# Kernel tuning notes

Measured on AMD Instinct MI355X. Metric: run time of the kernel, lower is better.

## Reference

```python
import jax, jax.numpy as jnp
import numpy as np

EPS = 1e-5
H, HD = 8, 32  # n_heads, head_dim


def layer_norm(x, w, b):
    mu = jnp.mean(x, axis=-1, keepdims=True)
    var = jnp.mean(jnp.square(x - mu), axis=-1, keepdims=True)
    return (x - mu) * jax.lax.rsqrt(var + EPS) * w + b


def setup_inputs() -> dict:
    key = jax.random.key(0)
    ks = jax.random.split(key, 6)
    S, N, Dm, Dz = 256, 512, 64, 128
    return {
        "m": jax.random.normal(ks[0], (1, S, N, Dm), jnp.float32),
        "z": jax.random.normal(ks[1], (1, N, N, Dz), jnp.float32),
        "m_norm_w": jnp.ones((Dm,), jnp.float32),
        "m_norm_b": jnp.zeros((Dm,), jnp.float32),
        "z_norm_w": jnp.ones((Dz,), jnp.float32),
        "z_norm_b": jnp.zeros((Dz,), jnp.float32),
        "Wm": jax.random.normal(ks[2], (Dm, H * HD), jnp.float32) * 0.05,
        "Wg": jax.random.normal(ks[3], (Dm, H * HD), jnp.float32) * 0.05,
        "Wz": jax.random.normal(ks[4], (Dz, H), jnp.float32) * 0.05,
        "Wo": jax.random.normal(ks[5], (H * HD, Dm), jnp.float32) * 0.05,
    }


def reference(m, z, m_norm_w, m_norm_b, z_norm_w, z_norm_b, Wm, Wg, Wz, Wo):
    m0 = m[0]  # [S, N, Dm]
    z0 = z[0]  # [N, N, Dz]
    Dm = m0.shape[-1]
    mn = layer_norm(m0, m_norm_w, m_norm_b)
    zn = layer_norm(z0, z_norm_w, z_norm_b)
    # per-head softmax bias from pair rep: b[h,i,j]
    b = jnp.einsum('ijc,ch->hij', zn, Wz)
    w = jax.nn.softmax(b, axis=-1)  # [H, N, N]
    # values and gates: [S, N, H, HD]
    v = jnp.einsum('snc,chk->snhk', mn, Wm.reshape(Dm, H, HD))
    g = jax.nn.sigmoid(jnp.einsum('snc,chk->snhk', mn, Wg.reshape(Dm, H, HD)))
    # weighted averaging over tokens j
    o = jnp.einsum('hij,sjhk->sihk', w, v)  # [S, N, H, HD]
    out = jnp.einsum('sihk,hkc->sic', o * g, Wo.reshape(H, HD, Dm))
    return out[None]  # [1, S, N, Dm]
```

## Files before the change

### kernel.cpp

```cpp
#include <hip/hip_runtime.h>


#define S_DIM 256
#define N_DIM 512
#define DM 64
#define DZ 128
#define NH 8
#define HD 32
#define HK 256
#define NP 8192
#define BKP 32
#define JT_N 16

typedef unsigned int   u32;
typedef unsigned short u16;
typedef __bf16 bf16x8 __attribute__((ext_vector_type(8)));
typedef float  f32x4  __attribute__((ext_vector_type(4)));
typedef u32    u32x4  __attribute__((ext_vector_type(4)));

__device__ __forceinline__ u16 f2bf(float f) {
  u32 u = __builtin_bit_cast(u32, f);
  return (u16)((u + 0x7FFFu + ((u >> 16) & 1u)) >> 16);
}
__device__ __forceinline__ float bf2f(u16 h) {
  u32 u = ((u32)h) << 16;
  return __builtin_bit_cast(float, u);
}
__device__ __forceinline__ u32 pack2(float a, float b) {
  return (u32)f2bf(a) | ((u32)f2bf(b) << 16);
}
__device__ __forceinline__ bf16x8 ld8(const u16* p) {
  return __builtin_bit_cast(bf16x8, *(const u32x4*)p);
}
__device__ __forceinline__ f32x4 mfma16(bf16x8 a, bf16x8 b, f32x4 c) {
  return __builtin_amdgcn_mfma_f32_16x16x32_bf16(a, b, c, 0, 0, 0);
}
__device__ __forceinline__ void gload_lds16(const void* gsrc, void* ldst) {
  __builtin_amdgcn_global_load_lds(
      (const __attribute__((address_space(1))) void*)gsrc,
      (__attribute__((address_space(3))) void*)ldst, 16, 0, 0);
}
__device__ __forceinline__ float fast_sigmoid(float x) {
  float r;
  asm("v_rcp_f32 %0, %1" : "=v"(r) : "v"(1.f + __expf(-x)));
  return r;
}
__device__ __forceinline__ int swz(int lin) { return lin ^ (((lin >> 7) & 3) << 4); }

#define BARRIER() do { asm volatile("" ::: "memory"); \
                       __builtin_amdgcn_s_barrier();  \
                       asm volatile("" ::: "memory"); } while (0)

__global__ __launch_bounds__(256) void k0_prep(
    const float* __restrict__ Wm, const float* __restrict__ Wg,
    const float* __restrict__ Wo, const float* __restrict__ znw,
    const float* __restrict__ znb, const float* __restrict__ Wz,
    u16* __restrict__ wmg, u16* __restrict__ wof,
    u16* __restrict__ wzf, float* __restrict__ t1c) {
  const int idx = blockIdx.x * 256 + threadIdx.x;
  if (idx < 32768) {
    const int t = idx & 7, lane = (idx >> 3) & 63, ks = (idx >> 9) & 1, cb = idx >> 10;
    const int c = cb * 16 + (lane & 15);
    const int k = ks * 32 + ((lane >> 4) & 3) * 8 + t;
    const float v = (c < HK) ? Wm[k * HK + c] : Wg[k * HK + (c - HK)];
    wmg[idx] = f2bf(v);
  } else if (idx < 32768 + 16384) {
    const int j = idx - 32768;
    const int t = j & 7, lane = (j >> 3) & 63, ks = (j >> 9) & 7, cb = j >> 12;
    const int c = cb * 16 + (lane & 15);
    const int hk = ks * 32 + ((lane >> 4) & 3) * 8 + t;
    wof[j] = f2bf(Wo[hk * DM + c]);
  } else if (idx < 49152 + 4096) {
    const int q = idx - 49152;
    const int t = q & 7, lane = (q >> 3) & 63, p = (q >> 9) & 1, ks = q >> 10;
    const int h = lane & 15;
    const int k = ks * 32 + ((lane >> 4) & 3) * 8 + t;
    u16 val = 0;
    if (h < NH) {
      const float wp = znw[k] * Wz[k * NH + h];
      const u16 hi = f2bf(wp);
      val = (p == 0) ? hi : f2bf(wp - bf2f(hi));
    }
    wzf[q] = val;
  } else if (idx < 49152 + 4096 + 16) {
    const int q = idx - 49152 - 4096;
    const int h = q & 7;
    float s = 0.f;
    for (int c = 0; c < DZ; ++c)
      s += ((q < 8) ? znw[c] : znb[c]) * Wz[c * NH + h];
    t1c[q] = s;
  }
}

__global__ __launch_bounds__(256) void k1a_bias(
    const float* __restrict__ z, const u16* __restrict__ wzf,
    const float* __restrict__ t1c, float* __restrict__ bws) {
  __shared__ float sB[NH][72];
  const int tid = threadIdx.x, lane = tid & 63, wv = tid >> 6;
  const int jb = blockIdx.x, i = blockIdx.y;
  const int jrow = jb * 64 + wv * 16 + (lane & 15);
  const float* zp = z + ((size_t)i * N_DIM + jrow) * DZ + ((lane >> 4) & 3) * 8;
  f32x4 acc = (f32x4){0.f, 0.f, 0.f, 0.f};
  float sum = 0.f, sq = 0.f;
  #pragma unroll
  for (int ks = 0; ks < 4; ++ks) {
    const float4 v0 = *(const float4*)(zp + ks * 32);
    const float4 v1 = *(const float4*)(zp + ks * 32 + 4);
    const float xs[8] = {v0.x, v0.y, v0.z, v0.w, v1.x, v1.y, v1.z, v1.w};
    bf16x8 zh, zl;
    #pragma unroll
    for (int t = 0; t < 8; ++t) {
      sum += xs[t]; sq += xs[t] * xs[t];
      const u16 h16 = f2bf(xs[t]);
      ((u16*)&zh)[t] = h16;
      ((u16*)&zl)[t] = f2bf(xs[t] - bf2f(h16));
    }
    const bf16x8 wh = ld8(wzf + (ks * 2 + 0) * 512 + lane * 8);
    const bf16x8 wl = ld8(wzf + (ks * 2 + 1) * 512 + lane * 8);
    acc = mfma16(zh, wh, acc);
    acc = mfma16(zl, wh, acc);
    acc = mfma16(zh, wl, acc);
  }
  sum += __shfl_xor(sum, 16, 64); sum += __shfl_xor(sum, 32, 64);
  sq  += __shfl_xor(sq, 16, 64);  sq  += __shfl_xor(sq, 32, 64);
  const float mu = sum * (1.f / DZ);
  const float rs = rsqrtf(sq * (1.f / DZ) - mu * mu + 1e-5f);
  const int h = lane & 15;
  const float t1 = t1c[h & 7], cst = t1c[8 + (h & 7)];
  #pragma unroll
  for (int rg = 0; rg < 4; ++rg) {
    const int r = ((lane >> 4) & 3) * 4 + rg;
    const float mur = __shfl(mu, r, 64);
    const float rsr = __shfl(rs, r, 64);
    const float bv = rsr * (acc[rg] - mur * t1) + cst;
    if (h < NH) sB[h][wv * 16 + r] = bv;
  }
  __syncthreads();
  #pragma unroll
  for (int q = 0; q < 2; ++q) {
    const int idx = tid + q * 256;
    const int hh = idx >> 6, jl = idx & 63;
    bws[((size_t)hh * N_DIM + i) * N_DIM + jb * 64 + jl] = sB[hh][jl];
  }
}

__global__ __launch_bounds__(256) void k1b_softmax(
    const float* __restrict__ bws, u16* __restrict__ wout) {
  const int tid = threadIdx.x, lane = tid & 63, wv = tid >> 6;
  const int row = blockIdx.x * 4 + wv;
  const int h = row >> 9, i = row & 511;
  const float* bp = bws + (size_t)row * N_DIM + lane * 8;
  const float4 v0 = *(const float4*)bp;
  const float4 v1 = *(const float4*)(bp + 4);
  float xs[8] = {v0.x, v0.y, v0.z, v0.w, v1.x, v1.y, v1.z, v1.w};
  float mx = xs[0];
  #pragma unroll
  for (int t = 1; t < 8; ++t) mx = fmaxf(mx, xs[t]);
  #pragma unroll
  for (int off = 32; off; off >>= 1) mx = fmaxf(mx, __shfl_xor(mx, off, 64));
  float sm = 0.f;
  #pragma unroll
  for (int t = 0; t < 8; ++t) { xs[t] = __expf(xs[t] - mx); sm += xs[t]; }
  #pragma unroll
  for (int off = 32; off; off >>= 1) sm += __shfl_xor(sm, off, 64);
  const float inv = 1.f / sm;
  u32x4 pk;
  pk[0] = pack2(xs[0] * inv, xs[1] * inv);
  pk[1] = pack2(xs[2] * inv, xs[3] * inv);
  pk[2] = pack2(xs[4] * inv, xs[5] * inv);
  pk[3] = pack2(xs[6] * inv, xs[7] * inv);
  *(u32x4*)(wout + (((size_t)(h * JT_N + (lane >> 2)) * N_DIM + i) << 5)
            + (lane & 3) * 8) = pk;
}

__global__ __launch_bounds__(256) void k2a_ln_m(
    const float* __restrict__ m, const float* __restrict__ mnw,
    const float* __restrict__ mnb, u16* __restrict__ mn) {
  __shared__ float sw[DM], sb[DM];
  const int tid = threadIdx.x;
  if (tid < DM) { sw[tid] = mnw[tid]; sb[tid] = mnb[tid]; }
  __syncthreads();
  const size_t r = (size_t)blockIdx.x * 256 + tid;
  const float4* mp = (const float4*)(m + r * DM);
  float4 arr[16];
  float sum = 0.f, sq = 0.f;
  #pragma unroll
  for (int q = 0; q < 16; ++q) {
    float4 v = mp[q]; arr[q] = v;
    sum += v.x + v.y + v.z + v.w;
    sq  += v.x * v.x + v.y * v.y + v.z * v.z + v.w * v.w;
  }
  const float mu = sum * (1.f / DM);
  const float rs = rsqrtf(sq * (1.f / DM) - mu * mu + 1e-5f);
  uint4* op = (uint4*)(mn + r * DM);
  #pragma unroll
  for (int q = 0; q < 8; ++q) {
    const float4 a = arr[2 * q], b = arr[2 * q + 1];
    const int c0 = q * 8;
    const float y0 = (a.x - mu) * rs * sw[c0 + 0] + sb[c0 + 0];
    const float y1 = (a.y - mu) * rs * sw[c0 + 1] + sb[c0 + 1];
    const float y2 = (a.z - mu) * rs * sw[c0 + 2] + sb[c0 + 2];
    const float y3 = (a.w - mu) * rs * sw[c0 + 3] + sb[c0 + 3];
    const float y4 = (b.x - mu) * rs * sw[c0 + 4] + sb[c0 + 4];
    const float y5 = (b.y - mu) * rs * sw[c0 + 5] + sb[c0 + 5];
    const float y6 = (b.z - mu) * rs * sw[c0 + 6] + sb[c0 + 6];
    const float y7 = (b.w - mu) * rs * sw[c0 + 7] + sb[c0 + 7];
    uint4 u;
    u.x = pack2(y0, y1); u.y = pack2(y2, y3);
    u.z = pack2(y4, y5); u.w = pack2(y6, y7);
    op[q] = u;
  }
}

__global__ __launch_bounds__(256) void k2b_proj(
    const u16* __restrict__ mn, const u16* __restrict__ wmg,
    u16* __restrict__ vf) {
  const int tid = threadIdx.x, lane = tid & 63, wv = tid >> 6;
  const int rbase = (blockIdx.x * 4 + wv) * 16;
  const u16* ap = mn + (size_t)(rbase + (lane & 15)) * DM + ((lane >> 4) & 3) * 8;
  const bf16x8 a0 = ld8(ap);
  const bf16x8 a1 = ld8(ap + 32);
  const u16* bp = wmg + lane * 8;
  const int r0 = rbase + ((lane >> 4) & 3) * 4;
  const int s0 = r0 >> 9;
  const int j0 = r0 & 511;

  f32x4 acc[16];
  #pragma unroll
  for (int cb = 0; cb < 16; ++cb) acc[cb] = (f32x4){0.f, 0.f, 0.f, 0.f};
  #pragma unroll
  for (int cb = 0; cb < 16; ++cb) {
    acc[cb] = mfma16(a0, ld8(bp + cb * 1024), acc[cb]);
    acc[cb] = mfma16(a1, ld8(bp + cb * 1024 + 512), acc[cb]);
  }
  #pragma unroll
  for (int cb = 0; cb < 16; ++cb) {
    const int c = cb * 16 + (lane & 15);
    const int h = c >> 5, k = c & 31;
    const int np = s0 * HD + k;
    const size_t idx = (((size_t)(h * JT_N + (j0 >> 5)) * NP + np) << 5) + (j0 & 31);
    ushort4 pk;
    pk.x = f2bf(acc[cb][0]); pk.y = f2bf(acc[cb][1]);
    pk.z = f2bf(acc[cb][2]); pk.w = f2bf(acc[cb][3]);
    *(ushort4*)(vf + idx) = pk;
  }
}

__global__ __launch_bounds__(256, 4) void k3_fused(
    const u16* __restrict__ wf, const u16* __restrict__ vf,
    const u16* __restrict__ mn, const u16* __restrict__ wmg,
    const u16* __restrict__ wof, float* __restrict__ out) {
  __shared__ __attribute__((aligned(16))) u16 ring[4][4096];
  const int tid = threadIdx.x, lane = tid & 63, wv = tid >> 6;
  const int q = (lane >> 4) & 3;
  const int wr = wv >> 1, wc = wv & 1;
  const int bid = blockIdx.x;
  const int xcd = bid & 7, j = bid >> 3;
  const int xt = xcd * 16 + (j >> 3);
  const int yt = j & 7;
  const int i0 = yt * 64;
  const int n0 = xt * 64;
  const int s  = xt * 2 + wc;

  const int sbA = wv * 1024;
  const int soA = swz(sbA + lane * 16);
  const int soB = swz(sbA + lane * 16);

  int offA[2], offB[2];
  #pragma unroll
  for (int f = 0; f < 2; ++f)
    offA[f] = swz((wr * 32 + f * 16 + (lane & 15)) * 64 + q * 16);
  #pragma unroll
  for (int f = 0; f < 2; ++f)
    offB[f] = 4096 + swz((wc * 32 + f * 16 + (lane & 15)) * 64 + q * 16);

  bf16x8 mnf[2][2];
  #pragma unroll
  for (int fi = 0; fi < 2; ++fi) {
    const u16* mp_ = mn + (size_t)(s * N_DIM + i0 + wr * 32 + fi * 16
                                   + (lane & 15)) * DM + q * 8;
    mnf[fi][0] = ld8(mp_);
    mnf[fi][1] = ld8(mp_ + 32);
  }

  f32x4 acc[2][2];
  f32x4 oacc[4][2];
  #pragma unroll
  for (int a = 0; a < 2; ++a)
    #pragma unroll
    for (int b = 0; b < 2; ++b) acc[a][b] = (f32x4){0.f, 0.f, 0.f, 0.f};
  #pragma unroll
  for (int a = 0; a < 4; ++a)
    #pragma unroll
    for (int b = 0; b < 2; ++b) oacc[a][b] = (f32x4){0.f, 0.f, 0.f, 0.f};

  const char* gA = (const char*)(wf + (size_t)i0 * 32);
  const char* gB = (const char*)(vf + (size_t)n0 * 32);

#define STAGE_P(pA_, pB_, slot)                                            \
  do {                                                                     \
    char* dA_ = (char*)&ring[(slot)][0];                                   \
    gload_lds16((pA_) + soA, dA_ + sbA);                                   \
    gload_lds16((pB_) + soB, dA_ + 4096 + sbA);                            \
  } while (0)

#define COMPUTE(slot)                                                      \
  do {                                                                     \
    const char* cS_ = (const char*)&ring[(slot)][0];                       \
    bf16x8 af_[2], bf_[2];                                                 \
    _Pragma("unroll")                                                      \
    for (int f = 0; f < 2; ++f) af_[f] = ld8((const u16*)(cS_ + offA[f])); \
    _Pragma("unroll")                                                      \
    for (int f = 0; f < 2; ++f) bf_[f] = ld8((const u16*)(cS_ + offB[f])); \
    __builtin_amdgcn_s_setprio(1);                                         \
    _Pragma("unroll")                                                      \
    for (int fi = 0; fi < 2; ++fi)                                         \
      _Pragma("unroll")                                                    \
      for (int fn = 0; fn < 2; ++fn)                                       \
        acc[fi][fn] = mfma16(bf_[fn], af_[fi], acc[fi][fn]);               \
    __builtin_amdgcn_s_setprio(0);                                         \
  } while (0)

#define INTERLUDE(hh)                                                      \
  do {                                                                     \
    bf16x8 wg_[2][2];                                                      \
    _Pragma("unroll")                                                      \
    for (int k2 = 0; k2 < 2; ++k2)                                         \
      _Pragma("unroll")                                                    \
      for (int kk = 0; kk < 2; ++kk)                                       \
        wg_[k2][kk] = ld8(wmg + ((16 + (hh) * 2 + k2) * 2 + kk) * 512 + lane * 8); \
    u16* bb_ = &ring[2][0] + wv * 1024;                                    \
    _Pragma("unroll")                                                      \
    for (int fi = 0; fi < 2; ++fi) {                                       \
      const int row_ = fi * 16 + (lane & 15);                              \
      const int sw_ = (row_ & 3) << 3;                                     \
      _Pragma("unroll")                                                    \
      for (int fn = 0; fn < 2; ++fn) {                                     \
        f32x4 ga_ = (f32x4){0.f, 0.f, 0.f, 0.f};                           \
        ga_ = mfma16(wg_[fn][0], mnf[fi][0], ga_);                         \
        ga_ = mfma16(wg_[fn][1], mnf[fi][1], ga_);                         \
        ushort4 pk_;                                                       \
        pk_.x = f2bf(acc[fi][fn][0] * fast_sigmoid(ga_[0]));               \
        pk_.y = f2bf(acc[fi][fn][1] * fast_sigmoid(ga_[1]));               \
        pk_.z = f2bf(acc[fi][fn][2] * fast_sigmoid(ga_[2]));               \
        pk_.w = f2bf(acc[fi][fn][3] * fast_sigmoid(ga_[3]));               \
        *(ushort4*)(bb_ + row_ * 32 + ((fn * 16 + q * 4) ^ sw_)) = pk_;    \
        acc[fi][fn] = (f32x4){0.f, 0.f, 0.f, 0.f};                         \
      }                                                                    \
    }                                                                      \
    asm volatile("s_waitcnt lgkmcnt(0)" ::: "memory");                     \
    __builtin_amdgcn_sched_barrier(0);                                     \
    bf16x8 ogf_[2], wo_[4];                                                \
    _Pragma("unroll")                                                      \
    for (int fi = 0; fi < 2; ++fi) {                                       \
      const int row_ = fi * 16 + (lane & 15);                              \
      ogf_[fi] = ld8(bb_ + row_ * 32 + ((q * 8) ^ ((row_ & 3) << 3)));     \
    }                                                                      \
    _Pragma("unroll")                                                      \
    for (int cn = 0; cn < 4; ++cn)                                         \
      wo_[cn] = ld8(wof + ((cn * 8 + (hh)) * 64 + lane) * 8);              \
    _Pragma("unroll")                                                      \
    for (int cn = 0; cn < 4; ++cn)                                         \
      _Pragma("unroll")                                                    \
      for (int fi = 0; fi < 2; ++fi)                                       \
        oacc[cn][fi] = mfma16(wo_[cn], ogf_[fi], oacc[cn][fi]);            \
  } while (0)

  STAGE_P(gA, gB, 0);
  STAGE_P(gA + 32768, gB + 524288, 1);

  for (int ho = 0; ho < 7; ++ho) {
    const char* pAh = gA + (size_t)(ho * 16) * 32768;
    const char* pBh = gB + (size_t)(ho * 16) * 524288;
    #pragma unroll
    for (int u = 0; u < 16; ++u) {
      asm volatile("s_waitcnt vmcnt(2)" ::: "memory");
      BARRIER();
      STAGE_P(pAh + (size_t)(u + 2) * 32768, pBh + (size_t)(u + 2) * 524288,
              (u + 2) & 3);
      COMPUTE(u & 3);
    }
    INTERLUDE(ho);
  }
  {
    const char* pAh = gA + (size_t)112 * 32768;
    const char* pBh = gB + (size_t)112 * 524288;
    #pragma unroll
    for (int u = 0; u < 14; ++u) {
      asm volatile("s_waitcnt vmcnt(2)" ::: "memory");
      BARRIER();
      STAGE_P(pAh + (size_t)(u + 2) * 32768, pBh + (size_t)(u + 2) * 524288,
              (u + 2) & 3);
      COMPUTE(u & 3);
    }
    asm volatile("s_waitcnt vmcnt(2)" ::: "memory");
    BARRIER();
    COMPUTE(2);
    asm volatile("s_waitcnt vmcnt(0)" ::: "memory");
    BARRIER();
    COMPUTE(3);
    INTERLUDE(7);
  }
#undef STAGE_P
#undef COMPUTE
#undef INTERLUDE

  #pragma unroll
  for (int cn = 0; cn < 4; ++cn) {
    #pragma unroll
    for (int fi = 0; fi < 2; ++fi) {
      float* op = out + (size_t)(s * N_DIM + i0 + wr * 32 + fi * 16
                                 + (lane & 15)) * DM + cn * 16 + q * 4;
      *(f32x4*)op = oacc[cn][fi];
    }
  }
}

extern "C" void kernel_launch(void* const* d_in, const int* in_sizes, int n_in,
                              void* d_out, int out_size, void* d_ws, size_t ws_size,
                              hipStream_t stream) {
  const float* m   = (const float*)d_in[0];
  const float* z   = (const float*)d_in[1];
  const float* mnw = (const float*)d_in[2];
  const float* mnb = (const float*)d_in[3];
  const float* znw = (const float*)d_in[4];
  const float* znb = (const float*)d_in[5];
  const float* Wm  = (const float*)d_in[6];
  const float* Wg  = (const float*)d_in[7];
  const float* Wz  = (const float*)d_in[8];
  const float* Wo  = (const float*)d_in[9];
  float* out = (float*)d_out;
  char* ws = (char*)d_ws;

  u16*   wbuf = (u16*)(ws);
  u16*   vf   = (u16*)(ws + ((size_t)4   << 20));
  u16*   mn   = (u16*)(ws + ((size_t)132 << 20));
  float* bws  = (float*)(ws + ((size_t)132 << 20));
  u16*   wmg  = (u16*)(ws + ((size_t)148 << 20));
  u16*   wof  = (u16*)(ws + ((size_t)148 << 20) + 65536);
  u16*   wzf  = (u16*)(ws + ((size_t)148 << 20) + 98304);
  float* t1c  = (float*)(ws + ((size_t)148 << 20) + 106496);

  k0_prep<<<209, 256, 0, stream>>>(Wm, Wg, Wo, znw, znb, Wz, wmg, wof, wzf, t1c);
  k1a_bias<<<dim3(8, 512), 256, 0, stream>>>(z, wzf, t1c, bws);
  k1b_softmax<<<1024, 256, 0, stream>>>(bws, wbuf);
  k2a_ln_m<<<512, 256, 0, stream>>>(m, mnw, mnb, mn);
  k2b_proj<<<2048, 256, 0, stream>>>(mn, wmg, vf);
  k3_fused<<<1024, 256, 0, stream>>>(wbuf, vf, mn, wmg, wof, out);
}
```

Measured before the change: 139.2 us.

## Load A operand directly into registers and deepen B LDS pipeline

```diff
diff --git a/kernel.cpp b/kernel.cpp
--- a/kernel.cpp
+++ b/kernel.cpp
@@ -250,7 +250,8 @@
     const u16* __restrict__ wf, const u16* __restrict__ vf,
     const u16* __restrict__ mn, const u16* __restrict__ wmg,
     const u16* __restrict__ wof, float* __restrict__ out) {
-  __shared__ __attribute__((aligned(16))) u16 ring[4][4096];
+  __shared__ __attribute__((aligned(16))) u16 ring[4][2048];
+  __shared__ __attribute__((aligned(16))) u16 sbnc[4][1024];
   const int tid = threadIdx.x, lane = tid & 63, wv = tid >> 6;
   const int q = (lane >> 4) & 3;
   const int wr = wv >> 1, wc = wv & 1;
@@ -262,17 +263,18 @@
   const int n0 = xt * 64;
   const int s  = xt * 2 + wc;
 
-  const int sbA = wv * 1024;
-  const int soA = swz(sbA + lane * 16);
-  const int soB = swz(sbA + lane * 16);
-
-  int offA[2], offB[2];
+  const int sbB = wv * 1024;
+  const int soB = swz(sbB + lane * 16);
+
+  int offB[2];
   #pragma unroll
   for (int f = 0; f < 2; ++f)
-    offA[f] = swz((wr * 32 + f * 16 + (lane & 15)) * 64 + q * 16);
+    offB[f] = swz((wc * 32 + f * 16 + (lane & 15)) * 64 + q * 16);
+
+  int aoff[2];
   #pragma unroll
   for (int f = 0; f < 2; ++f)
-    offB[f] = 4096 + swz((wc * 32 + f * 16 + (lane & 15)) * 64 + q * 16);
+    aoff[f] = (wr * 32 + f * 16 + (lane & 15)) * 64 + q * 16;
 
   bf16x8 mnf[2][2];
   #pragma unroll
@@ -297,19 +299,21 @@
   const char* gA = (const char*)(wf + (size_t)i0 * 32);
   const char* gB = (const char*)(vf + (size_t)n0 * 32);
 
-#define STAGE_P(pA_, pB_, slot)                                            \
+  bf16x8 aF[2][2];
+
+#define LOADA(tt, buf)                                                     \
   do {                                                                     \
-    char* dA_ = (char*)&ring[(slot)][0];                                   \
-    gload_lds16((pA_) + soA, dA_ + sbA);                                   \
-    gload_lds16((pB_) + soB, dA_ + 4096 + sbA);                            \
+    aF[buf][0] = ld8((const u16*)(gA + (size_t)(tt) * 32768 + aoff[0]));   \
+    aF[buf][1] = ld8((const u16*)(gA + (size_t)(tt) * 32768 + aoff[1]));   \
   } while (0)
 
-#define COMPUTE(slot)                                                      \
+#define STAGEB(tt, slot)                                                   \
+  gload_lds16(gB + (size_t)(tt) * 524288 + soB, (char*)&ring[(slot)][0] + sbB)
+
+#define COMPUTE(slot, buf)                                                 \
   do {                                                                     \
     const char* cS_ = (const char*)&ring[(slot)][0];                       \
-    bf16x8 af_[2], bf_[2];                                                 \
-    _Pragma("unroll")                                                      \
-    for (int f = 0; f < 2; ++f) af_[f] = ld8((const u16*)(cS_ + offA[f])); \
+    bf16x8 bf_[2];                                                         \
     _Pragma("unroll")                                                      \
     for (int f = 0; f < 2; ++f) bf_[f] = ld8((const u16*)(cS_ + offB[f])); \
     __builtin_amdgcn_s_setprio(1);                                         \
@@ -317,7 +321,7 @@
     for (int fi = 0; fi < 2; ++fi)                                         \
       _Pragma("unroll")                                                    \
       for (int fn = 0; fn < 2; ++fn)                                       \
-        acc[fi][fn] = mfma16(bf_[fn], af_[fi], acc[fi][fn]);               \
+        acc[fi][fn] = mfma16(bf_[fn], aF[buf][fi], acc[fi][fn]);           \
     __builtin_amdgcn_s_setprio(0);                                         \
   } while (0)
 
@@ -329,7 +333,7 @@
       _Pragma("unroll")                                                    \
       for (int kk = 0; kk < 2; ++kk)                                       \
         wg_[k2][kk] = ld8(wmg + ((16 + (hh) * 2 + k2) * 2 + kk) * 512 + lane * 8); \
-    u16* bb_ = &ring[2][0] + wv * 1024;                                    \
+    u16* bb_ = &sbnc[wv][0];                                               \
     _Pragma("unroll")                                                      \
     for (int fi = 0; fi < 2; ++fi) {                                       \
       const int row_ = fi * 16 + (lane & 15);                              \
@@ -366,42 +370,50 @@
         oacc[cn][fi] = mfma16(wo_[cn], ogf_[fi], oacc[cn][fi]);            \
   } while (0)
 
-  STAGE_P(gA, gB, 0);
-  STAGE_P(gA + 32768, gB + 524288, 1);
+  STAGEB(0, 0);
+  STAGEB(1, 1);
+  STAGEB(2, 2);
+  __builtin_amdgcn_sched_barrier(0);
+  LOADA(0, 0);
+  LOADA(1, 1);
 
   for (int ho = 0; ho < 7; ++ho) {
-    const char* pAh = gA + (size_t)(ho * 16) * 32768;
-    const char* pBh = gB + (size_t)(ho * 16) * 524288;
+    const size_t tb = (size_t)ho * 16;
     #pragma unroll
     for (int u = 0; u < 16; ++u) {
-      asm volatile("s_waitcnt vmcnt(2)" ::: "memory");
+      asm volatile("s_waitcnt vmcnt(6)" ::: "memory");
       BARRIER();
-      STAGE_P(pAh + (size_t)(u + 2) * 32768, pBh + (size_t)(u + 2) * 524288,
-              (u + 2) & 3);
-      COMPUTE(u & 3);
+      LOADA(tb + u + 1, (u + 1) & 1);
+      STAGEB(tb + u + 3, (u + 3) & 3);
+      COMPUTE(u & 3, u & 1);
     }
     INTERLUDE(ho);
   }
   {
-    const char* pAh = gA + (size_t)112 * 32768;
-    const char* pBh = gB + (size_t)112 * 524288;
-    #pragma unroll
-    for (int u = 0; u < 14; ++u) {
-      asm volatile("s_waitcnt vmcnt(2)" ::: "memory");
+    const size_t tb = 112;
+    #pragma unroll
+    for (int u = 0; u < 13; ++u) {
+      asm volatile("s_waitcnt vmcnt(6)" ::: "memory");
       BARRIER();
-      STAGE_P(pAh + (size_t)(u + 2) * 32768, pBh + (size_t)(u + 2) * 524288,
-              (u + 2) & 3);
-      COMPUTE(u & 3);
+      LOADA(tb + u + 1, (u + 1) & 1);
+      STAGEB(tb + u + 3, (u + 3) & 3);
+      COMPUTE(u & 3, u & 1);
     }
+    asm volatile("s_waitcnt vmcnt(4)" ::: "memory");
+    BARRIER();
+    LOADA(126, 0);
+    COMPUTE(1, 1);
+    asm volatile("s_waitcnt vmcnt(3)" ::: "memory");
+    BARRIER();
+    LOADA(127, 1);
+    COMPUTE(2, 0);
     asm volatile("s_waitcnt vmcnt(2)" ::: "memory");
     BARRIER();
-    COMPUTE(2);
-    asm volatile("s_waitcnt vmcnt(0)" ::: "memory");
-    BARRIER();
-    COMPUTE(3);
+    COMPUTE(3, 1);
     INTERLUDE(7);
   }
-#undef STAGE_P
+#undef LOADA
+#undef STAGEB
 #undef COMPUTE
 #undef INTERLUDE
 
```

Result: slower. 171.3 us (+23.1%).

## Fuse pair-bias with softmax and m layernorm with value projection

Applied to the files above, without the earlier changes.

```diff
diff --git a/kernel.cpp b/kernel.cpp
--- a/kernel.cpp
+++ b/kernel.cpp
@@ -92,134 +92,122 @@
   }
 }
 
-__global__ __launch_bounds__(256) void k1a_bias(
+__global__ __launch_bounds__(256) void k1_fused(
     const float* __restrict__ z, const u16* __restrict__ wzf,
-    const float* __restrict__ t1c, float* __restrict__ bws) {
-  __shared__ float sB[NH][72];
+    const float* __restrict__ t1c, u16* __restrict__ wout) {
+  __shared__ float sB[NH][N_DIM + 4];
   const int tid = threadIdx.x, lane = tid & 63, wv = tid >> 6;
-  const int jb = blockIdx.x, i = blockIdx.y;
-  const int jrow = jb * 64 + wv * 16 + (lane & 15);
-  const float* zp = z + ((size_t)i * N_DIM + jrow) * DZ + ((lane >> 4) & 3) * 8;
-  f32x4 acc = (f32x4){0.f, 0.f, 0.f, 0.f};
+  const int i = blockIdx.x;
+  const int h16 = lane & 15;
+  const float t1 = t1c[h16 & 7], cst = t1c[8 + (h16 & 7)];
+
+  for (int jj = 0; jj < 8; ++jj) {
+    const int jrow = jj * 64 + wv * 16 + (lane & 15);
+    const float* zp = z + ((size_t)i * N_DIM + jrow) * DZ + ((lane >> 4) & 3) * 8;
+    f32x4 acc = (f32x4){0.f, 0.f, 0.f, 0.f};
+    float sum = 0.f, sq = 0.f;
+    #pragma unroll
+    for (int ks = 0; ks < 4; ++ks) {
+      const float4 v0 = *(const float4*)(zp + ks * 32);
+      const float4 v1 = *(const float4*)(zp + ks * 32 + 4);
+      const float xs[8] = {v0.x, v0.y, v0.z, v0.w, v1.x, v1.y, v1.z, v1.w};
+      bf16x8 zh, zl;
+      #pragma unroll
+      for (int t = 0; t < 8; ++t) {
+        sum += xs[t]; sq += xs[t] * xs[t];
+        const u16 hv = f2bf(xs[t]);
+        ((u16*)&zh)[t] = hv;
+        ((u16*)&zl)[t] = f2bf(xs[t] - bf2f(hv));
+      }
+      const bf16x8 wh = ld8(wzf + (ks * 2 + 0) * 512 + lane * 8);
+      const bf16x8 wl = ld8(wzf + (ks * 2 + 1) * 512 + lane * 8);
+      acc = mfma16(zh, wh, acc);
+      acc = mfma16(zl, wh, acc);
+      acc = mfma16(zh, wl, acc);
+    }
+    sum += __shfl_xor(sum, 16, 64); sum += __shfl_xor(sum, 32, 64);
+    sq  += __shfl_xor(sq, 16, 64);  sq  += __shfl_xor(sq, 32, 64);
+    const float mu = sum * (1.f / DZ);
+    const float rs = rsqrtf(sq * (1.f / DZ) - mu * mu + 1e-5f);
+    #pragma unroll
+    for (int rg = 0; rg < 4; ++rg) {
+      const int r = ((lane >> 4) & 3) * 4 + rg;
+      const float mur = __shfl(mu, r, 64);
+      const float rsr = __shfl(rs, r, 64);
+      const float bv = rsr * (acc[rg] - mur * t1) + cst;
+      if (h16 < NH) sB[h16][jj * 64 + wv * 16 + r] = bv;
+    }
+  }
+  __syncthreads();
+
+  #pragma unroll
+  for (int hh = 0; hh < 2; ++hh) {
+    const int h = wv * 2 + hh;
+    const float* bp = &sB[h][lane * 8];
+    const float4 v0 = *(const float4*)bp;
+    const float4 v1 = *(const float4*)(bp + 4);
+    float xs[8] = {v0.x, v0.y, v0.z, v0.w, v1.x, v1.y, v1.z, v1.w};
+    float mx = xs[0];
+    #pragma unroll
+    for (int t = 1; t < 8; ++t) mx = fmaxf(mx, xs[t]);
+    #pragma unroll
+    for (int off = 32; off; off >>= 1) mx = fmaxf(mx, __shfl_xor(mx, off, 64));
+    float sm = 0.f;
+    #pragma unroll
+    for (int t = 0; t < 8; ++t) { xs[t] = __expf(xs[t] - mx); sm += xs[t]; }
+    #pragma unroll
+    for (int off = 32; off; off >>= 1) sm += __shfl_xor(sm, off, 64);
+    const float inv = 1.f / sm;
+    u32x4 pk;
+    pk[0] = pack2(xs[0] * inv, xs[1] * inv);
+    pk[1] = pack2(xs[2] * inv, xs[3] * inv);
+    pk[2] = pack2(xs[4] * inv, xs[5] * inv);
+    pk[3] = pack2(xs[6] * inv, xs[7] * inv);
+    *(u32x4*)(wout + (((size_t)(h * JT_N + (lane >> 2)) * N_DIM + i) << 5)
+              + (lane & 3) * 8) = pk;
+  }
+}
+
+__global__ __launch_bounds__(256) void k2_fused(
+    const float* __restrict__ m, const float* __restrict__ mnw,
+    const float* __restrict__ mnb, const u16* __restrict__ wmg,
+    u16* __restrict__ mn, u16* __restrict__ vf) {
+  __shared__ float swt[DM], sbs[DM];
+  const int tid = threadIdx.x, lane = tid & 63, wv = tid >> 6;
+  if (tid < DM) { swt[tid] = mnw[tid]; sbs[tid] = mnb[tid]; }
+  __syncthreads();
+  const int q = (lane >> 4) & 3;
+  const int rbase = (blockIdx.x * 4 + wv) * 16;
+  const int r = rbase + (lane & 15);
+
+  const float* mp = m + (size_t)r * DM + q * 8;
+  const float4 va = *(const float4*)(mp);
+  const float4 vb = *(const float4*)(mp + 4);
+  const float4 vc = *(const float4*)(mp + 32);
+  const float4 vd = *(const float4*)(mp + 36);
+  const float x0[8] = {va.x, va.y, va.z, va.w, vb.x, vb.y, vb.z, vb.w};
+  const float x1[8] = {vc.x, vc.y, vc.z, vc.w, vd.x, vd.y, vd.z, vd.w};
   float sum = 0.f, sq = 0.f;
   #pragma unroll
-  for (int ks = 0; ks < 4; ++ks) {
-    const float4 v0 = *(const float4*)(zp + ks * 32);
-    const float4 v1 = *(const float4*)(zp + ks * 32 + 4);
-    const float xs[8] = {v0.x, v0.y, v0.z, v0.w, v1.x, v1.y, v1.z, v1.w};
-    bf16x8 zh, zl;
-    #pragma unroll
-    for (int t = 0; t < 8; ++t) {
-      sum += xs[t]; sq += xs[t] * xs[t];
-      const u16 h16 = f2bf(xs[t]);
-      ((u16*)&zh)[t] = h16;
-      ((u16*)&zl)[t] = f2bf(xs[t] - bf2f(h16));
-    }
-    const bf16x8 wh = ld8(wzf + (ks * 2 + 0) * 512 + lane * 8);
-    const bf16x8 wl = ld8(wzf + (ks * 2 + 1) * 512 + lane * 8);
-    acc = mfma16(zh, wh, acc);
-    acc = mfma16(zl, wh, acc);
-    acc = mfma16(zh, wl, acc);
+  for (int t = 0; t < 8; ++t) {
+    sum += x0[t] + x1[t];
+    sq  += x0[t] * x0[t] + x1[t] * x1[t];
   }
   sum += __shfl_xor(sum, 16, 64); sum += __shfl_xor(sum, 32, 64);
   sq  += __shfl_xor(sq, 16, 64);  sq  += __shfl_xor(sq, 32, 64);
-  const float mu = sum * (1.f / DZ);
-  const float rs = rsqrtf(sq * (1.f / DZ) - mu * mu + 1e-5f);
-  const int h = lane & 15;
-  const float t1 = t1c[h & 7], cst = t1c[8 + (h & 7)];
-  #pragma unroll
-  for (int rg = 0; rg < 4; ++rg) {
-    const int r = ((lane >> 4) & 3) * 4 + rg;
-    const float mur = __shfl(mu, r, 64);
-    const float rsr = __shfl(rs, r, 64);
-    const float bv = rsr * (acc[rg] - mur * t1) + cst;
-    if (h < NH) sB[h][wv * 16 + r] = bv;
-  }
-  __syncthreads();
-  #pragma unroll
-  for (int q = 0; q < 2; ++q) {
-    const int idx = tid + q * 256;
-    const int hh = idx >> 6, jl = idx & 63;
-    bws[((size_t)hh * N_DIM + i) * N_DIM + jb * 64 + jl] = sB[hh][jl];
-  }
-}
-
-__global__ __launch_bounds__(256) void k1b_softmax(
-    const float* __restrict__ bws, u16* __restrict__ wout) {
-  const int tid = threadIdx.x, lane = tid & 63, wv = tid >> 6;
-  const int row = blockIdx.x * 4 + wv;
-  const int h = row >> 9, i = row & 511;
-  const float* bp = bws + (size_t)row * N_DIM + lane * 8;
-  const float4 v0 = *(const float4*)bp;
-  const float4 v1 = *(const float4*)(bp + 4);
-  float xs[8] = {v0.x, v0.y, v0.z, v0.w, v1.x, v1.y, v1.z, v1.w};
-  float mx = xs[0];
-  #pragma unroll
-  for (int t = 1; t < 8; ++t) mx = fmaxf(mx, xs[t]);
-  #pragma unroll
-  for (int off = 32; off; off >>= 1) mx = fmaxf(mx, __shfl_xor(mx, off, 64));
-  float sm = 0.f;
-  #pragma unroll
-  for (int t = 0; t < 8; ++t) { xs[t] = __expf(xs[t] - mx); sm += xs[t]; }
-  #pragma unroll
-  for (int off = 32; off; off >>= 1) sm += __shfl_xor(sm, off, 64);
-  const float inv = 1.f / sm;
-  u32x4 pk;
-  pk[0] = pack2(xs[0] * inv, xs[1] * inv);
-  pk[1] = pack2(xs[2] * inv, xs[3] * inv);
-  pk[2] = pack2(xs[4] * inv, xs[5] * inv);
-  pk[3] = pack2(xs[6] * inv, xs[7] * inv);
-  *(u32x4*)(wout + (((size_t)(h * JT_N + (lane >> 2)) * N_DIM + i) << 5)
-            + (lane & 3) * 8) = pk;
-}
-
-__global__ __launch_bounds__(256) void k2a_ln_m(
-    const float* __restrict__ m, const float* __restrict__ mnw,
-    const float* __restrict__ mnb, u16* __restrict__ mn) {
-  __shared__ float sw[DM], sb[DM];
-  const int tid = threadIdx.x;
-  if (tid < DM) { sw[tid] = mnw[tid]; sb[tid] = mnb[tid]; }
-  __syncthreads();
-  const size_t r = (size_t)blockIdx.x * 256 + tid;
-  const float4* mp = (const float4*)(m + r * DM);
-  float4 arr[16];
-  float sum = 0.f, sq = 0.f;
-  #pragma unroll
-  for (int q = 0; q < 16; ++q) {
-    float4 v = mp[q]; arr[q] = v;
-    sum += v.x + v.y + v.z + v.w;
-    sq  += v.x * v.x + v.y * v.y + v.z * v.z + v.w * v.w;
-  }
   const float mu = sum * (1.f / DM);
   const float rs = rsqrtf(sq * (1.f / DM) - mu * mu + 1e-5f);
-  uint4* op = (uint4*)(mn + r * DM);
-  #pragma unroll
-  for (int q = 0; q < 8; ++q) {
-    const float4 a = arr[2 * q], b = arr[2 * q + 1];
-    const int c0 = q * 8;
-    const float y0 = (a.x - mu) * rs * sw[c0 + 0] + sb[c0 + 0];
-    const float y1 = (a.y - mu) * rs * sw[c0 + 1] + sb[c0 + 1];
-    const float y2 = (a.z - mu) * rs * sw[c0 + 2] + sb[c0 + 2];
-    const float y3 = (a.w - mu) * rs * sw[c0 + 3] + sb[c0 + 3];
-    const float y4 = (b.x - mu) * rs * sw[c0 + 4] + sb[c0 + 4];
-    const float y5 = (b.y - mu) * rs * sw[c0 + 5] + sb[c0 + 5];
-    const float y6 = (b.z - mu) * rs * sw[c0 + 6] + sb[c0 + 6];
-    const float y7 = (b.w - mu) * rs * sw[c0 + 7] + sb[c0 + 7];
-    uint4 u;
-    u.x = pack2(y0, y1); u.y = pack2(y2, y3);
-    u.z = pack2(y4, y5); u.w = pack2(y6, y7);
-    op[q] = u;
-  }
-}
-
-__global__ __launch_bounds__(256) void k2b_proj(
-    const u16* __restrict__ mn, const u16* __restrict__ wmg,
-    u16* __restrict__ vf) {
-  const int tid = threadIdx.x, lane = tid & 63, wv = tid >> 6;
-  const int rbase = (blockIdx.x * 4 + wv) * 16;
-  const u16* ap = mn + (size_t)(rbase + (lane & 15)) * DM + ((lane >> 4) & 3) * 8;
-  const bf16x8 a0 = ld8(ap);
-  const bf16x8 a1 = ld8(ap + 32);
+
+  bf16x8 a0, a1;
+  #pragma unroll
+  for (int t = 0; t < 8; ++t) {
+    const int c0 = q * 8 + t, c1 = q * 8 + 32 + t;
+    ((u16*)&a0)[t] = f2bf((x0[t] - mu) * rs * swt[c0] + sbs[c0]);
+    ((u16*)&a1)[t] = f2bf((x1[t] - mu) * rs * swt[c1] + sbs[c1]);
+  }
+  *(u32x4*)(mn + (size_t)r * DM + q * 8)      = __builtin_bit_cast(u32x4, a0);
+  *(u32x4*)(mn + (size_t)r * DM + q * 8 + 32) = __builtin_bit_cast(u32x4, a1);
+
   const u16* bp = wmg + lane * 8;
   const int r0 = rbase + ((lane >> 4) & 3) * 4;
   const int s0 = r0 >> 9;
@@ -435,16 +423,13 @@
   u16*   wbuf = (u16*)(ws);
   u16*   vf   = (u16*)(ws + ((size_t)4   << 20));
   u16*   mn   = (u16*)(ws + ((size_t)132 << 20));
-  float* bws  = (float*)(ws + ((size_t)132 << 20));
   u16*   wmg  = (u16*)(ws + ((size_t)148 << 20));
   u16*   wof  = (u16*)(ws + ((size_t)148 << 20) + 65536);
   u16*   wzf  = (u16*)(ws + ((size_t)148 << 20) + 98304);
   float* t1c  = (float*)(ws + ((size_t)148 << 20) + 106496);
 
   k0_prep<<<209, 256, 0, stream>>>(Wm, Wg, Wo, znw, znb, Wz, wmg, wof, wzf, t1c);
-  k1a_bias<<<dim3(8, 512), 256, 0, stream>>>(z, wzf, t1c, bws);
-  k1b_softmax<<<1024, 256, 0, stream>>>(bws, wbuf);
-  k2a_ln_m<<<512, 256, 0, stream>>>(m, mnw, mnb, mn);
-  k2b_proj<<<2048, 256, 0, stream>>>(mn, wmg, vf);
+  k1_fused<<<512, 256, 0, stream>>>(z, wzf, t1c, wbuf);
+  k2_fused<<<2048, 256, 0, stream>>>(m, mnw, mnb, wmg, mn, vf);
   k3_fused<<<1024, 256, 0, stream>>>(wbuf, vf, mn, wmg, wof, out);
 }
```

New measurement: 131.3 us. -5.7%, faster.
